# Optimization experiments

Measured on AMD Instinct MI355X. Metric: run time of the kernel, lower is better.

The kernel has to match this reference:

```python
import jax, jax.numpy as jnp
import numpy as np

V = 100000
NNZ = 1600000
B = 4
C_IN = 64
C_HID = 128
C_OUT = 64
K = 4
BN_EPS = 1e-5


def cheb_conv(x, rows, cols, vals, W, b):
    # x: (B, Cin, V); W: (K, Cin, Cout); b: (Cout,)
    Bn, Cin, Vn = x.shape
    Kn = W.shape[0]

    def spmm(y):  # y: (V, F) -> L @ y via edge-list scatter-add
        return jax.ops.segment_sum(vals[:, None] * y[cols], rows, num_segments=Vn)

    x0 = jnp.transpose(x, (2, 0, 1)).reshape(Vn, Bn * Cin)  # (V, B*Cin)
    xs = [x0]
    if Kn > 1:
        x1 = spmm(x0)
        xs.append(x1)
        for _ in range(2, Kn):
            x2 = 2.0 * spmm(x1) - x0  # Chebyshev recurrence
            xs.append(x2)
            x0, x1 = x1, x2
    Xk = jnp.stack(xs, 0).reshape(Kn, Vn, Bn, Cin)  # (K, V, B, Cin)
    out = jnp.einsum('kvbi,kio->bov', Xk, W)  # (B, Cout, V)
    return out + b[None, :, None]


def batch_norm(x, gamma, beta):
    # BatchNorm1d on (B, C, V): stats over (B, V), biased variance (training mode)
    mean = jnp.mean(x, axis=(0, 2), keepdims=True)
    var = jnp.mean(jnp.square(x - mean), axis=(0, 2), keepdims=True)
    xn = (x - mean) * jax.lax.rsqrt(var + BN_EPS)
    return xn * gamma[None, :, None] + beta[None, :, None]


def setup_inputs() -> dict:
    key = jax.random.key(0)
    ks = jax.random.split(key, 8)
    x = jax.random.normal(ks[0], (B, C_IN, V), dtype=jnp.float32)
    lap_rows = jax.random.randint(ks[1], (NNZ,), 0, V, dtype=jnp.int32)
    lap_cols = jax.random.randint(ks[2], (NNZ,), 0, V, dtype=jnp.int32)
    # scale so the effective Laplacian spectral norm is ~O(1) (Chebyshev assumes rescaled L)
    lap_vals = jax.random.normal(ks[3], (NNZ,), dtype=jnp.float32) * 0.01
    w1 = jax.random.normal(ks[4], (K, C_IN, C_HID), dtype=jnp.float32) * (1.0 / np.sqrt(K * C_IN))
    b1 = jnp.zeros((C_HID,), dtype=jnp.float32)
    bn_gamma = jnp.ones((C_HID,), dtype=jnp.float32)
    bn_beta = jnp.zeros((C_HID,), dtype=jnp.float32)
    w2 = jax.random.normal(ks[5], (K, C_HID, C_OUT), dtype=jnp.float32) * (1.0 / np.sqrt(K * C_HID))
    b2 = jnp.zeros((C_OUT,), dtype=jnp.float32)
    return {"x": x, "lap_rows": lap_rows, "lap_cols": lap_cols, "lap_vals": lap_vals,
            "w1": w1, "b1": b1, "bn_gamma": bn_gamma, "bn_beta": bn_beta,
            "w2": w2, "b2": b2}


def reference(x, lap_rows, lap_cols, lap_vals, w1, b1, bn_gamma, bn_beta, w2, b2):
    out = cheb_conv(x, lap_rows, lap_cols, lap_vals, w1, b1)
    out = jax.nn.relu(out)
    out = batch_norm(out, bn_gamma, bn_beta)
    out = cheb_conv(out, lap_rows, lap_cols, lap_vals, w2, b2)
    # in_channels == out_channels -> resizer is Identity
    return jax.nn.relu(out + x)
```

## Files before the change

### kernel.cpp

```cpp
#include <hip/hip_runtime.h>

#define V 100000
#define NNZ 1600000

typedef unsigned short ushort_t;
typedef unsigned int uint_t;
typedef __attribute__((ext_vector_type(4))) float f32x4;
typedef __attribute__((ext_vector_type(8))) short bf16x8;

__device__ __forceinline__ float bf2f(ushort_t u) {
    union { uint_t i; float f; } x; x.i = ((uint_t)u) << 16; return x.f;
}
__device__ __forceinline__ ushort_t f2bf(float f) {
    union { float f; uint_t i; } x; x.f = f;
    uint_t u = x.i;
    return (ushort_t)((u + 0x7fffu + ((u >> 16) & 1u)) >> 16);
}
__device__ __forceinline__ float blo(uint_t u) {
    union { uint_t i; float f; } x; x.i = u << 16; return x.f;
}
__device__ __forceinline__ float bhi(uint_t u) {
    union { uint_t i; float f; } x; x.i = u & 0xffff0000u; return x.f;
}
__device__ __forceinline__ uint_t pk(float a, float b) {
    return (uint_t)f2bf(a) | ((uint_t)f2bf(b) << 16);
}
__device__ __forceinline__ void unpack8(uint4 u, float* f) {
    f[0] = blo(u.x); f[1] = bhi(u.x); f[2] = blo(u.y); f[3] = bhi(u.y);
    f[4] = blo(u.z); f[5] = bhi(u.z); f[6] = blo(u.w); f[7] = bhi(u.w);
}
__device__ __forceinline__ uint4 pack8(const float* f) {
    uint4 u;
    u.x = pk(f[0], f[1]); u.y = pk(f[2], f[3]);
    u.z = pk(f[4], f[5]); u.w = pk(f[6], f[7]);
    return u;
}

__global__ void diag_k(float* __restrict__ out, float code) {
    if (threadIdx.x == 0 && blockIdx.x == 0) out[0] = code;
}

__global__ __launch_bounds__(256) void pack_x0_k(const float* __restrict__ x,
                                                 ushort_t* __restrict__ x0) {
    __shared__ float tile[32][33];
    int v0 = blockIdx.x * 32, j0 = blockIdx.y * 32;
    int tx = threadIdx.x & 31, ty = threadIdx.x >> 5;
    for (int jj = ty; jj < 32; jj += 8)
        tile[jj][tx] = x[(size_t)(j0 + jj) * V + v0 + tx];
    __syncthreads();
    for (int vv = ty; vv < 32; vv += 8)
        x0[(size_t)(v0 + vv) * 256 + j0 + tx] = f2bf(tile[tx][vv]);
}

__global__ __launch_bounds__(256) void prep_w_k(const float* __restrict__ w1,
                                                const float* __restrict__ w2,
                                                ushort_t* __restrict__ wp1,
                                                ushort_t* __restrict__ wp2) {
    int idx = blockIdx.x * 256 + threadIdx.x;
    if (idx < 32768) {
        int f = idx;
        int j = f & 7, ch = (f >> 3) & 127, q = (f >> 10) & 3, kb = (f >> 12) & 3, L = (f >> 14) & 1;
        int k = kb * 32 + q * 8 + j;
        int t = L * 2 + (k >> 6), i = k & 63;
        wp1[idx] = f2bf(w1[((size_t)t * 64 + i) * 128 + ch]);
    } else {
        int f = idx - 32768;
        int j = f & 7, o = (f >> 3) & 63, q = (f >> 9) & 3, kb = (f >> 11) & 3, t = (f >> 13) & 3;
        int k = kb * 32 + q * 8 + j;
        wp2[f] = f2bf(w2[((size_t)t * 128 + k) * 64 + o]);
    }
}

__global__ __launch_bounds__(256) void hist_k(const int* __restrict__ rows,
                                              int* __restrict__ counts) {
    int e = blockIdx.x * 256 + threadIdx.x;
    atomicAdd(&counts[rows[e]], 1);
}

__global__ __launch_bounds__(256) void scan1_k(const int* __restrict__ counts,
                                               int* __restrict__ bsums) {
    __shared__ int sd[256];
    int t = threadIdx.x;
    int v = blockIdx.x * 256 + t;
    sd[t] = (v < V) ? counts[v] : 0;
    __syncthreads();
    for (int s = 128; s > 0; s >>= 1) {
        if (t < s) sd[t] += sd[t + s];
        __syncthreads();
    }
    if (t == 0) bsums[blockIdx.x] = sd[0];
}

__global__ __launch_bounds__(512) void scan2_k(int* __restrict__ bsums, int nb) {
    __shared__ int sd[512];
    int t = threadIdx.x;
    int v = (t < nb) ? bsums[t] : 0;
    sd[t] = v;
    __syncthreads();
    for (int off = 1; off < 512; off <<= 1) {
        int a = (t >= off) ? sd[t - off] : 0;
        __syncthreads();
        sd[t] += a;
        __syncthreads();
    }
    if (t < nb) bsums[t] = sd[t] - v;
}

__global__ __launch_bounds__(256) void scan3_k(const int* __restrict__ counts,
                                               const int* __restrict__ bsums,
                                               int* __restrict__ rowptr,
                                               int* __restrict__ cursor) {
    __shared__ int sd[256];
    int t = threadIdx.x;
    int v = blockIdx.x * 256 + t;
    int c = (v < V) ? counts[v] : 0;
    sd[t] = c;
    __syncthreads();
    for (int off = 1; off < 256; off <<= 1) {
        int a = (t >= off) ? sd[t - off] : 0;
        __syncthreads();
        sd[t] += a;
        __syncthreads();
    }
    if (v < V) {
        int start = bsums[blockIdx.x] + sd[t] - c;
        rowptr[v] = start;
        cursor[v] = start;
    }
    if (v == 0) rowptr[V] = NNZ;
}

__global__ __launch_bounds__(256) void scatter_k(const int* __restrict__ rows,
                                                 const int* __restrict__ cols,
                                                 const float* __restrict__ vals,
                                                 int* __restrict__ cursor,
                                                 int2* __restrict__ edges) {
    int e = blockIdx.x * 256 + threadIdx.x;
    int r = rows[e];
    int pos = atomicAdd(&cursor[r], 1);
    edges[pos] = make_int2(cols[e], __float_as_int(vals[e]));
}

__global__ __launch_bounds__(256) void spmm_wave(const int* __restrict__ rowptr,
                                                 const int2* __restrict__ edges,
                                                 const ushort_t* __restrict__ y,
                                                 const ushort_t* __restrict__ z,
                                                 float alpha, float beta,
                                                 ushort_t* __restrict__ out) {
    int v = __builtin_amdgcn_readfirstlane((blockIdx.x * 256 + threadIdx.x) >> 6);
    if (v >= V) return;
    int l = threadIdx.x & 63;
    const ushort_t* yl = y + l * 4;

    float a0 = 0.f, a1 = 0.f, a2 = 0.f, a3 = 0.f;
    int e0 = __builtin_amdgcn_readfirstlane(rowptr[v]);
    int e1 = __builtin_amdgcn_readfirstlane(rowptr[v + 1]);
    int e = e0;
    for (; e + 8 <= e1; e += 8) {
        int2 ed[8];
#pragma unroll
        for (int i = 0; i < 8; ++i) ed[i] = edges[e + i];
        uint2 u[8];
#pragma unroll
        for (int i = 0; i < 8; ++i) u[i] = *(const uint2*)(yl + (size_t)ed[i].x * 256);
#pragma unroll
        for (int i = 0; i < 8; ++i) {
            float wv = __int_as_float(ed[i].y);
            a0 += wv * blo(u[i].x);
            a1 += wv * bhi(u[i].x);
            a2 += wv * blo(u[i].y);
            a3 += wv * bhi(u[i].y);
        }
    }
    auto masked4 = [&](int base, int cnt) {
        int2 ed[4];
#pragma unroll
        for (int i = 0; i < 4; ++i) ed[i] = edges[i < cnt ? base + i : e0];
        uint2 u[4];
#pragma unroll
        for (int i = 0; i < 4; ++i) u[i] = *(const uint2*)(yl + (size_t)ed[i].x * 256);
#pragma unroll
        for (int i = 0; i < 4; ++i) {
            float wv = (i < cnt) ? __int_as_float(ed[i].y) : 0.f;
            a0 += wv * blo(u[i].x);
            a1 += wv * bhi(u[i].x);
            a2 += wv * blo(u[i].y);
            a3 += wv * bhi(u[i].y);
        }
    };
    int rem = e1 - e;
    if (rem > 0) masked4(e, rem > 4 ? 4 : rem);
    if (rem > 4) masked4(e + 4, rem - 4);

    float r0 = alpha * a0, r1 = alpha * a1, r2 = alpha * a2, r3 = alpha * a3;
    if (z) {
        uint2 t = *(const uint2*)(z + (size_t)v * 256 + l * 4);
        r0 += beta * blo(t.x);
        r1 += beta * bhi(t.x);
        r2 += beta * blo(t.y);
        r3 += beta * bhi(t.y);
    }
    uint2 st;
    st.x = (uint_t)f2bf(r0) | ((uint_t)f2bf(r1) << 16);
    st.y = (uint_t)f2bf(r2) | ((uint_t)f2bf(r3) << 16);
    *(uint2*)(out + (size_t)v * 256 + l * 4) = st;
}

__global__ __launch_bounds__(256) void gemm1_mfma(const ushort_t* __restrict__ t0,
                                                  const ushort_t* __restrict__ t1,
                                                  const ushort_t* __restrict__ wp,
                                                  const float* __restrict__ b1,
                                                  ushort_t* __restrict__ rb,
                                                  int first, int last) {
    __shared__ float smem[64 * 66];
    int tid = threadIdx.x;
    int l = tid & 63, w = tid >> 6;
    int q = l >> 4, n16 = l & 15;
    int b = blockIdx.y;
    int v0 = blockIdx.x * 64;
    int vrow = v0 + w * 16 + n16;
    int vc = vrow < V ? vrow : V - 1;

    f32x4 acc[8];
#pragma unroll
    for (int ct = 0; ct < 8; ++ct) acc[ct] = (f32x4){0.f, 0.f, 0.f, 0.f};

#pragma unroll
    for (int kb = 0; kb < 4; ++kb) {
        const ushort_t* tab = (kb < 2) ? t0 : t1;
        bf16x8 a = *(const bf16x8*)(tab + (size_t)vc * 256 + b * 64 + (kb & 1) * 32 + q * 8);
#pragma unroll
        for (int ct = 0; ct < 8; ++ct) {
            bf16x8 bf = *(const bf16x8*)(wp + (size_t)(((kb * 4 + q) * 128) + ct * 16 + n16) * 8);
            acc[ct] = __builtin_amdgcn_mfma_f32_16x16x32_bf16(a, bf, acc[ct], 0, 0, 0);
        }
    }

    int row_d = tid >> 3;
    int c8 = tid & 7;
#pragma unroll
    for (int h = 0; h < 2; ++h) {
        if (h) __syncthreads();
#pragma unroll
        for (int ct = 0; ct < 4; ++ct)
#pragma unroll
            for (int r = 0; r < 4; ++r)
                smem[(w * 16 + q * 4 + r) * 66 + ct * 16 + n16] = acc[h * 4 + ct][r];
        __syncthreads();

        int ch0 = h * 64 + c8 * 8;
        float bc[8];
        if (last) {
#pragma unroll
            for (int j = 0; j < 8; ++j) bc[j] = b1[ch0 + j];
        }
#pragma unroll
        for (int k = 0; k < 2; ++k) {
            int row = row_d + k * 32;
            int v = v0 + row;
            bool valid = v < V;
            float vals[8];
#pragma unroll
            for (int j = 0; j < 8; ++j) vals[j] = smem[row * 66 + c8 * 8 + j];
            ushort_t* p = rb + (size_t)(valid ? v : 0) * 512 + b * 128 + ch0;
            if (!first && valid) {
                uint4 old = *(const uint4*)p;
                float of[8];
                unpack8(old, of);
#pragma unroll
                for (int j = 0; j < 8; ++j) vals[j] += of[j];
            }
            if (last) {
#pragma unroll
                for (int j = 0; j < 8; ++j) vals[j] = fmaxf(vals[j] + bc[j], 0.f);
            }
            if (valid) *(uint4*)p = pack8(vals);
        }
    }
}

__global__ __launch_bounds__(256) void stats_k(const ushort_t* __restrict__ rb,
                                               float* __restrict__ stats) {
    __shared__ float s_sum[128], s_sq[128];
    int tid = threadIdx.x;
    if (tid < 128) { s_sum[tid] = 0.f; s_sq[tid] = 0.f; }
    __syncthreads();
    int g = tid & 15, t16 = tid >> 4;
    float cs[8], cq[8];
#pragma unroll
    for (int j = 0; j < 8; ++j) { cs[j] = 0.f; cq[j] = 0.f; }
    for (int idx = blockIdx.x * 16 + t16; idx < V * 4; idx += 256 * 16) {
        int v = idx >> 2, bb = idx & 3;
        uint4 u = *(const uint4*)(rb + (size_t)v * 512 + bb * 128 + g * 8);
        float f[8];
        unpack8(u, f);
#pragma unroll
        for (int j = 0; j < 8; ++j) { cs[j] += f[j]; cq[j] += f[j] * f[j]; }
    }
#pragma unroll
    for (int j = 0; j < 8; ++j) {
        cs[j] += __shfl_xor(cs[j], 16); cs[j] += __shfl_xor(cs[j], 32);
        cq[j] += __shfl_xor(cq[j], 16); cq[j] += __shfl_xor(cq[j], 32);
    }
    if ((tid & 63) < 16) {
#pragma unroll
        for (int j = 0; j < 8; ++j) {
            atomicAdd(&s_sum[g * 8 + j], cs[j]);
            atomicAdd(&s_sq[g * 8 + j], cq[j]);
        }
    }
    __syncthreads();
    if (tid < 128) {
        atomicAdd(&stats[tid], s_sum[tid]);
        atomicAdd(&stats[128 + tid], s_sq[tid]);
    }
}

__global__ void finalize_k(const float* __restrict__ stats,
                           const float* __restrict__ gamma,
                           const float* __restrict__ beta,
                           float* __restrict__ ss) {
    int c = threadIdx.x;
    float n = (float)(4 * V);
    float mean = stats[c] / n;
    float var = stats[128 + c] / n - mean * mean;
    float inv = rsqrtf(var + 1e-5f);
    float sc = gamma[c] * inv;
    ss[c] = sc;
    ss[128 + c] = beta[c] - mean * sc;
}

__global__ __launch_bounds__(256) void gemmC_mfma(const ushort_t* __restrict__ rb,
                                                  const ushort_t* __restrict__ wp,
                                                  const ushort_t* __restrict__ S,
                                                  const float* __restrict__ ss,
                                                  ushort_t* __restrict__ P) {
    __shared__ float s_ss[256];
    __shared__ float smem[64 * 66];
    int tid = threadIdx.x;
    s_ss[tid] = ss[tid];
    __syncthreads();
    int l = tid & 63, w = tid >> 6;
    int q = l >> 4, n16 = l & 15;
    int b = blockIdx.y;
    int v0 = blockIdx.x * 64;
    int vrow = v0 + w * 16 + n16;
    int vc = vrow < V ? vrow : V - 1;

    f32x4 acc[4];
#pragma unroll
    for (int ct = 0; ct < 4; ++ct) acc[ct] = (f32x4){0.f, 0.f, 0.f, 0.f};

#pragma unroll
    for (int kb = 0; kb < 4; ++kb) {
        int chl = kb * 32 + q * 8;
        bf16x8 a = *(const bf16x8*)(rb + (size_t)vc * 512 + b * 128 + chl);
#pragma unroll
        for (int j = 0; j < 8; ++j) {
            float f = bf2f((ushort_t)a[j]) * s_ss[chl + j] + s_ss[128 + chl + j];
            a[j] = (short)f2bf(f);
        }
#pragma unroll
        for (int ct = 0; ct < 4; ++ct) {
            bf16x8 bf = *(const bf16x8*)(wp + (size_t)(((kb * 4 + q) * 64) + ct * 16 + n16) * 8);
            acc[ct] = __builtin_amdgcn_mfma_f32_16x16x32_bf16(a, bf, acc[ct], 0, 0, 0);
        }
    }

#pragma unroll
    for (int ct = 0; ct < 4; ++ct)
#pragma unroll
        for (int r = 0; r < 4; ++r)
            smem[(w * 16 + q * 4 + r) * 66 + ct * 16 + n16] = acc[ct][r];
    __syncthreads();

#pragma unroll
    for (int k = 0; k < 2; ++k) {
        int seg = tid + k * 256;
        int row = seg >> 3;
        int o0 = (seg & 7) * 8;
        int v = v0 + row;
        if (v >= V) continue;
        float vals[8];
#pragma unroll
        for (int j = 0; j < 8; ++j) vals[j] = smem[row * 66 + o0 + j];
        size_t idx = (size_t)v * 256 + b * 64 + o0;
        if (S) {
            uint4 sv = *(const uint4*)(S + idx);
            float sf[8];
            unpack8(sv, sf);
#pragma unroll
            for (int j = 0; j < 8; ++j) vals[j] += sf[j];
        }
        *(uint4*)(P + idx) = pack8(vals);
    }
}

__global__ __launch_bounds__(256) void gemm2_final(const ushort_t* __restrict__ rb,
                                                   const ushort_t* __restrict__ wp,
                                                   const ushort_t* __restrict__ Tb,
                                                   const float* __restrict__ b2,
                                                   const float* __restrict__ xres,
                                                   const float* __restrict__ ss,
                                                   float* __restrict__ out) {
    __shared__ float s_ss[256];
    __shared__ float s_b2[64];
    __shared__ uint_t s_tb[128 * 36];
    int tid = threadIdx.x;
    s_ss[tid] = ss[tid];
    if (tid < 64) s_b2[tid] = b2[tid];
    int l = tid & 63, w = tid >> 6;
    int q = l >> 4, n16 = l & 15;
    int b = blockIdx.y;
    int v0 = blockIdx.x * 128;

#pragma unroll
    for (int k = 0; k < 4; ++k) {
        int seg = tid + k * 256;
        int row = seg >> 3, c = seg & 7;
        uint4 t = make_uint4(0u, 0u, 0u, 0u);
        if (v0 + row < V) t = *(const uint4*)(Tb + (size_t)(v0 + row) * 256 + b * 64 + c * 8);
        *(uint4*)&s_tb[row * 36 + c * 4] = t;
    }
    __syncthreads();

    f32x4 acc[4][2];
#pragma unroll
    for (int rt = 0; rt < 4; ++rt)
#pragma unroll
        for (int c = 0; c < 2; ++c) acc[rt][c] = (f32x4){0.f, 0.f, 0.f, 0.f};

    int vcol[2];
#pragma unroll
    for (int c = 0; c < 2; ++c) {
        int v = v0 + (w * 2 + c) * 16 + n16;
        vcol[c] = v < V ? v : V - 1;
    }

#pragma unroll
    for (int kb = 0; kb < 4; ++kb) {
        int chl = kb * 32 + q * 8;
        bf16x8 bfr[2];
#pragma unroll
        for (int c = 0; c < 2; ++c) {
            bf16x8 t = *(const bf16x8*)(rb + (size_t)vcol[c] * 512 + b * 128 + chl);
#pragma unroll
            for (int j = 0; j < 8; ++j) {
                float f = bf2f((ushort_t)t[j]) * s_ss[chl + j] + s_ss[128 + chl + j];
                t[j] = (short)f2bf(f);
            }
            bfr[c] = t;
        }
#pragma unroll
        for (int rt = 0; rt < 4; ++rt) {
            bf16x8 af = *(const bf16x8*)(wp + (size_t)(((kb * 4 + q) * 64) + rt * 16 + n16) * 8);
#pragma unroll
            for (int c = 0; c < 2; ++c)
                acc[rt][c] = __builtin_amdgcn_mfma_f32_16x16x32_bf16(af, bfr[c], acc[rt][c], 0, 0, 0);
        }
    }

#pragma unroll
    for (int rt = 0; rt < 4; ++rt)
#pragma unroll
        for (int c = 0; c < 2; ++c) {
            int vl = (w * 2 + c) * 16 + n16;
            int v = v0 + vl;
            bool valid = v < V;
            int vv = valid ? v : 0;
#pragma unroll
            for (int r = 0; r < 4; ++r) {
                int o = rt * 16 + q * 4 + r;
                uint_t pr = s_tb[vl * 36 + rt * 8 + q * 2 + (r >> 1)];
                float tb = (r & 1) ? bhi(pr) : blo(pr);
                size_t idx = (size_t)(b * 64 + o) * V + vv;
                float val = acc[rt][c][r] + tb + s_b2[o] + xres[idx];
                if (valid) out[idx] = fmaxf(val, 0.f);
            }
        }
}

extern "C" void kernel_launch(void* const* d_in, const int* in_sizes, int n_in,
                              void* d_out, int out_size, void* d_ws, size_t ws_size,
                              hipStream_t stream) {
    const float* x = (const float*)d_in[0];
    const int* lap_rows = (const int*)d_in[1];
    const int* lap_cols = (const int*)d_in[2];
    const float* lap_vals = (const float*)d_in[3];
    const float* w1 = (const float*)d_in[4];
    const float* b1 = (const float*)d_in[5];
    const float* bn_gamma = (const float*)d_in[6];
    const float* bn_beta = (const float*)d_in[7];
    const float* w2 = (const float*)d_in[8];
    const float* b2 = (const float*)d_in[9];
    float* out = (float*)d_out;

    char* ws = (char*)d_ws;
    size_t off = 0;
    auto alloc = [&](size_t bytes) {
        size_t r = off;
        off = (off + bytes + 255) & ~(size_t)255;
        return r;
    };
    size_t reg1_off = alloc((size_t)V * 512 * 2);
    size_t rb_off   = alloc((size_t)V * 512 * 2);
    size_t sc_off   = alloc((size_t)V * 256 * 2);
    size_t rp_off   = alloc((size_t)(V + 1) * 4);
    size_t cur_off  = alloc((size_t)V * 4);
    size_t ed_off   = alloc((size_t)NNZ * 8);
    size_t st_off   = alloc(256 * 4);
    size_t ss_off   = alloc(256 * 4);
    size_t bs_off   = alloc(512 * 4);
    size_t wp1_off  = alloc(32768 * 2);
    size_t wp2_off  = alloc(32768 * 2);

    if (ws_size < off) {
        diag_k<<<1, 64, 0, stream>>>(out, 1000.f + (float)(ws_size >> 20));
        return;
    }

    ushort_t* slotA = (ushort_t*)(ws + reg1_off);
    ushort_t* slotB = slotA + (size_t)V * 256;
    ushort_t* slotC = (ushort_t*)(ws + sc_off);
    ushort_t* rb = (ushort_t*)(ws + rb_off);
    int* rowptr = (int*)(ws + rp_off);
    int* cursor = (int*)(ws + cur_off);
    int2* edges = (int2*)(ws + ed_off);
    float* stats = (float*)(ws + st_off);
    float* ss = (float*)(ws + ss_off);
    int* bsums = (int*)(ws + bs_off);
    ushort_t* wp1 = (ushort_t*)(ws + wp1_off);
    ushort_t* wp2 = (ushort_t*)(ws + wp2_off);

    const int NB = (V + 255) / 256;
    const int SG = (V + 3) / 4;
    const ushort_t* nullu = (const ushort_t*)nullptr;

    hipMemsetAsync(cursor, 0, (size_t)V * 4, stream);
    hipMemsetAsync(stats, 0, 256 * 4, stream);

    pack_x0_k<<<dim3(V / 32, 8), 256, 0, stream>>>(x, slotA);
    prep_w_k<<<256, 256, 0, stream>>>(w1, w2, wp1, wp2);
    hist_k<<<NNZ / 256, 256, 0, stream>>>(lap_rows, cursor);
    scan1_k<<<NB, 256, 0, stream>>>(cursor, bsums);
    scan2_k<<<1, 512, 0, stream>>>(bsums, NB);
    scan3_k<<<NB, 256, 0, stream>>>(cursor, bsums, rowptr, cursor);
    scatter_k<<<NNZ / 256, 256, 0, stream>>>(lap_rows, lap_cols, lap_vals, cursor, edges);

    dim3 g1((V + 63) / 64, 4);
    dim3 g2((V + 127) / 128, 4);

    spmm_wave<<<SG, 256, 0, stream>>>(rowptr, edges, slotA, nullu, 1.f, 0.f, slotB);
    gemm1_mfma<<<g1, 256, 0, stream>>>(slotA, slotB, wp1, b1, rb, 1, 0);
    spmm_wave<<<SG, 256, 0, stream>>>(rowptr, edges, slotB, slotA, 2.f, -1.f, slotA);
    spmm_wave<<<SG, 256, 0, stream>>>(rowptr, edges, slotA, slotB, 2.f, -1.f, slotB);
    gemm1_mfma<<<g1, 256, 0, stream>>>(slotA, slotB, wp1 + 16384, b1, rb, 0, 1);

    stats_k<<<256, 256, 0, stream>>>(rb, stats);
    finalize_k<<<1, 128, 0, stream>>>(stats, bn_gamma, bn_beta, ss);

    gemmC_mfma<<<g1, 256, 0, stream>>>(rb, wp2 + 3 * 8192, nullu, ss, slotA);
    spmm_wave<<<SG, 256, 0, stream>>>(rowptr, edges, slotA, nullu, 2.f, 0.f, slotB);
    gemmC_mfma<<<g1, 256, 0, stream>>>(rb, wp2 + 2 * 8192, slotB, ss, slotC);
    spmm_wave<<<SG, 256, 0, stream>>>(rowptr, edges, slotC, slotA, 2.f, -1.f, slotA);
    gemmC_mfma<<<g1, 256, 0, stream>>>(rb, wp2 + 1 * 8192, slotA, ss, slotB);
    spmm_wave<<<SG, 256, 0, stream>>>(rowptr, edges, slotB, slotC, 1.f, -1.f, slotC);
    gemm2_final<<<g2, 256, 0, stream>>>(rb, wp2, slotC, b2, x, ss, out);
}
```

Measured before the change: 1.430 ms.

## Stage GEMM A-operands through swizzled LDS with coalesced loads; shrink final tile

```diff
diff --git a/kernel.cpp b/kernel.cpp
--- a/kernel.cpp
+++ b/kernel.cpp
@@ -212,29 +212,45 @@
                                                   const float* __restrict__ b1,
                                                   ushort_t* __restrict__ rb,
                                                   int first, int last) {
-    __shared__ float smem[64 * 66];
+    __shared__ uint4 s_buf[1088];
+    uint4* s_a = s_buf;
+    float* smem = (float*)s_buf;
     int tid = threadIdx.x;
     int l = tid & 63, w = tid >> 6;
     int q = l >> 4, n16 = l & 15;
     int b = blockIdx.y;
     int v0 = blockIdx.x * 64;
-    int vrow = v0 + w * 16 + n16;
-    int vc = vrow < V ? vrow : V - 1;
+
+    {
+        int row = tid >> 3, c = tid & 7;
+        int row2 = row + 32;
+        int va = v0 + row;  va = va < V ? va : V - 1;
+        int vb = v0 + row2; vb = vb < V ? vb : V - 1;
+        size_t ga = (size_t)va * 256 + b * 64 + c * 8;
+        size_t gb = (size_t)vb * 256 + b * 64 + c * 8;
+        s_a[row * 8 + (c ^ (row & 7))] = *(const uint4*)(t0 + ga);
+        s_a[row2 * 8 + (c ^ (row2 & 7))] = *(const uint4*)(t0 + gb);
+        s_a[512 + row * 8 + (c ^ (row & 7))] = *(const uint4*)(t1 + ga);
+        s_a[512 + row2 * 8 + (c ^ (row2 & 7))] = *(const uint4*)(t1 + gb);
+    }
+    __syncthreads();
 
     f32x4 acc[8];
 #pragma unroll
     for (int ct = 0; ct < 8; ++ct) acc[ct] = (f32x4){0.f, 0.f, 0.f, 0.f};
 
+    int arow = w * 16 + n16;
 #pragma unroll
     for (int kb = 0; kb < 4; ++kb) {
-        const ushort_t* tab = (kb < 2) ? t0 : t1;
-        bf16x8 a = *(const bf16x8*)(tab + (size_t)vc * 256 + b * 64 + (kb & 1) * 32 + q * 8);
+        int T = kb >> 1;
+        bf16x8 a = *(const bf16x8*)&s_a[T * 512 + arow * 8 + (((kb & 1) * 4 + q) ^ (arow & 7))];
 #pragma unroll
         for (int ct = 0; ct < 8; ++ct) {
             bf16x8 bf = *(const bf16x8*)(wp + (size_t)(((kb * 4 + q) * 128) + ct * 16 + n16) * 8);
             acc[ct] = __builtin_amdgcn_mfma_f32_16x16x32_bf16(a, bf, acc[ct], 0, 0, 0);
         }
     }
+    __syncthreads();
 
     int row_d = tid >> 3;
     int c8 = tid & 7;
@@ -336,25 +352,34 @@
                                                   const float* __restrict__ ss,
                                                   ushort_t* __restrict__ P) {
     __shared__ float s_ss[256];
-    __shared__ float smem[64 * 66];
+    __shared__ uint4 s_buf[1088];
+    uint4* s_rb = s_buf;
+    float* smem = (float*)s_buf;
     int tid = threadIdx.x;
     s_ss[tid] = ss[tid];
-    __syncthreads();
     int l = tid & 63, w = tid >> 6;
     int q = l >> 4, n16 = l & 15;
     int b = blockIdx.y;
     int v0 = blockIdx.x * 64;
-    int vrow = v0 + w * 16 + n16;
-    int vc = vrow < V ? vrow : V - 1;
+
+#pragma unroll
+    for (int k = 0; k < 4; ++k) {
+        int idx = tid + k * 256;
+        int row = idx >> 4, c = idx & 15;
+        int v = v0 + row; v = v < V ? v : V - 1;
+        s_rb[row * 16 + (c ^ (row & 7))] = *(const uint4*)(rb + (size_t)v * 512 + b * 128 + c * 8);
+    }
+    __syncthreads();
 
     f32x4 acc[4];
 #pragma unroll
     for (int ct = 0; ct < 4; ++ct) acc[ct] = (f32x4){0.f, 0.f, 0.f, 0.f};
 
+    int arow = w * 16 + n16;
 #pragma unroll
     for (int kb = 0; kb < 4; ++kb) {
         int chl = kb * 32 + q * 8;
-        bf16x8 a = *(const bf16x8*)(rb + (size_t)vc * 512 + b * 128 + chl);
+        bf16x8 a = *(const bf16x8*)&s_rb[arow * 16 + ((kb * 4 + q) ^ (arow & 7))];
 #pragma unroll
         for (int j = 0; j < 8; ++j) {
             float f = bf2f((ushort_t)a[j]) * s_ss[chl + j] + s_ss[128 + chl + j];
@@ -366,6 +391,7 @@
             acc[ct] = __builtin_amdgcn_mfma_f32_16x16x32_bf16(a, bf, acc[ct], 0, 0, 0);
         }
     }
+    __syncthreads();
 
 #pragma unroll
     for (int ct = 0; ct < 4; ++ct)
@@ -405,78 +431,67 @@
                                                    float* __restrict__ out) {
     __shared__ float s_ss[256];
     __shared__ float s_b2[64];
-    __shared__ uint_t s_tb[128 * 36];
+    __shared__ uint_t s_tb[64 * 36];
+    __shared__ uint4 s_rb[1024];
     int tid = threadIdx.x;
     s_ss[tid] = ss[tid];
     if (tid < 64) s_b2[tid] = b2[tid];
     int l = tid & 63, w = tid >> 6;
     int q = l >> 4, n16 = l & 15;
     int b = blockIdx.y;
-    int v0 = blockIdx.x * 128;
-
-#pragma unroll
-    for (int k = 0; k < 4; ++k) {
+    int v0 = blockIdx.x * 64;
+
+#pragma unroll
+    for (int k = 0; k < 2; ++k) {
         int seg = tid + k * 256;
         int row = seg >> 3, c = seg & 7;
         uint4 t = make_uint4(0u, 0u, 0u, 0u);
         if (v0 + row < V) t = *(const uint4*)(Tb + (size_t)(v0 + row) * 256 + b * 64 + c * 8);
         *(uint4*)&s_tb[row * 36 + c * 4] = t;
     }
-    __syncthreads();
-
-    f32x4 acc[4][2];
-#pragma unroll
-    for (int rt = 0; rt < 4; ++rt)
-#pragma unroll
-        for (int c = 0; c < 2; ++c) acc[rt][c] = (f32x4){0.f, 0.f, 0.f, 0.f};
-
-    int vcol[2];
-#pragma unroll
-    for (int c = 0; c < 2; ++c) {
-        int v = v0 + (w * 2 + c) * 16 + n16;
-        vcol[c] = v < V ? v : V - 1;
-    }
-
+#pragma unroll
+    for (int k = 0; k < 4; ++k) {
+        int idx = tid + k * 256;
+        int row = idx >> 4, c = idx & 15;
+        int v = v0 + row; v = v < V ? v : V - 1;
+        s_rb[row * 16 + (c ^ (row & 7))] = *(const uint4*)(rb + (size_t)v * 512 + b * 128 + c * 8);
+    }
+    __syncthreads();
+
+    f32x4 acc[4];
+#pragma unroll
+    for (int rt = 0; rt < 4; ++rt) acc[rt] = (f32x4){0.f, 0.f, 0.f, 0.f};
+
+    int vl = w * 16 + n16;
 #pragma unroll
     for (int kb = 0; kb < 4; ++kb) {
         int chl = kb * 32 + q * 8;
-        bf16x8 bfr[2];
-#pragma unroll
-        for (int c = 0; c < 2; ++c) {
-            bf16x8 t = *(const bf16x8*)(rb + (size_t)vcol[c] * 512 + b * 128 + chl);
-#pragma unroll
-            for (int j = 0; j < 8; ++j) {
-                float f = bf2f((ushort_t)t[j]) * s_ss[chl + j] + s_ss[128 + chl + j];
-                t[j] = (short)f2bf(f);
-            }
-            bfr[c] = t;
+        bf16x8 t = *(const bf16x8*)&s_rb[vl * 16 + ((kb * 4 + q) ^ (vl & 7))];
+#pragma unroll
+        for (int j = 0; j < 8; ++j) {
+            float f = bf2f((ushort_t)t[j]) * s_ss[chl + j] + s_ss[128 + chl + j];
+            t[j] = (short)f2bf(f);
         }
 #pragma unroll
         for (int rt = 0; rt < 4; ++rt) {
             bf16x8 af = *(const bf16x8*)(wp + (size_t)(((kb * 4 + q) * 64) + rt * 16 + n16) * 8);
-#pragma unroll
-            for (int c = 0; c < 2; ++c)
-                acc[rt][c] = __builtin_amdgcn_mfma_f32_16x16x32_bf16(af, bfr[c], acc[rt][c], 0, 0, 0);
-        }
-    }
-
+            acc[rt] = __builtin_amdgcn_mfma_f32_16x16x32_bf16(af, t, acc[rt], 0, 0, 0);
+        }
+    }
+
+    int v = v0 + vl;
+    bool valid = v < V;
+    int vv = valid ? v : 0;
 #pragma unroll
     for (int rt = 0; rt < 4; ++rt)
 #pragma unroll
-        for (int c = 0; c < 2; ++c) {
-            int vl = (w * 2 + c) * 16 + n16;
-            int v = v0 + vl;
-            bool valid = v < V;
-            int vv = valid ? v : 0;
-#pragma unroll
-            for (int r = 0; r < 4; ++r) {
-                int o = rt * 16 + q * 4 + r;
-                uint_t pr = s_tb[vl * 36 + rt * 8 + q * 2 + (r >> 1)];
-                float tb = (r & 1) ? bhi(pr) : blo(pr);
-                size_t idx = (size_t)(b * 64 + o) * V + vv;
-                float val = acc[rt][c][r] + tb + s_b2[o] + xres[idx];
-                if (valid) out[idx] = fmaxf(val, 0.f);
-            }
+        for (int r = 0; r < 4; ++r) {
+            int o = rt * 16 + q * 4 + r;
+            uint_t pr = s_tb[vl * 36 + rt * 8 + q * 2 + (r >> 1)];
+            float tb = (r & 1) ? bhi(pr) : blo(pr);
+            size_t idx = (size_t)(b * 64 + o) * V + vv;
+            float val = acc[rt][r] + tb + s_b2[o] + xres[idx];
+            if (valid) out[idx] = fmaxf(val, 0.f);
         }
 }
 
@@ -548,7 +563,6 @@
     scatter_k<<<NNZ / 256, 256, 0, stream>>>(lap_rows, lap_cols, lap_vals, cursor, edges);
 
     dim3 g1((V + 63) / 64, 4);
-    dim3 g2((V + 127) / 128, 4);
 
     spmm_wave<<<SG, 256, 0, stream>>>(rowptr, edges, slotA, nullu, 1.f, 0.f, slotB);
     gemm1_mfma<<<g1, 256, 0, stream>>>(slotA, slotB, wp1, b1, rb, 1, 0);
@@ -565,5 +579,5 @@
     spmm_wave<<<SG, 256, 0, stream>>>(rowptr, edges, slotC, slotA, 2.f, -1.f, slotA);
     gemmC_mfma<<<g1, 256, 0, stream>>>(rb, wp2 + 1 * 8192, slotA, ss, slotB);
     spmm_wave<<<SG, 256, 0, stream>>>(rowptr, edges, slotB, slotC, 1.f, -1.f, slotC);
-    gemm2_final<<<g2, 256, 0, stream>>>(rb, wp2, slotC, b2, x, ss, out);
-}
+    gemm2_final<<<g1, 256, 0, stream>>>(rb, wp2, slotC, b2, x, ss, out);
+}
```

Result: no change. 1.407 ms (-1.6%).
